# Performance work log

Measured on AMD Instinct MI355X. Metric: run time of the kernel, lower is better.

Reference implementation:

```python
import jax, jax.numpy as jnp
import numpy as np

NEG_SLOPE = 0.01  # torch leaky_relu default

def _leaky_relu(x):
    return jnp.where(x >= 0, x, NEG_SLOPE * x)

def setup_inputs() -> dict:
    key = jax.random.key(0)
    ks = jax.random.split(key, 12)
    n_drug, n_disease, n_edges, d = 10000, 10000, 1000000, 100
    inp = {
        "x_drug": jax.random.normal(ks[0], (n_drug, d), dtype=jnp.float32),
        "x_disease": jax.random.normal(ks[1], (n_disease, d), dtype=jnp.float32),
        "edge_label_index": jax.random.randint(ks[2], (2, n_edges), 0, n_drug, dtype=jnp.int64),
        "W1": jax.random.normal(ks[3], (200, 128), dtype=jnp.float32) * 0.07,
        "b1": jax.random.normal(ks[4], (128,), dtype=jnp.float32) * 0.01,
        "W2": jax.random.normal(ks[5], (128, 32), dtype=jnp.float32) * 0.09,
        "b2": jax.random.normal(ks[6], (32,), dtype=jnp.float32) * 0.01,
        "W3": jax.random.normal(ks[7], (32, 16), dtype=jnp.float32) * 0.18,
        "b3": jax.random.normal(ks[8], (16,), dtype=jnp.float32) * 0.01,
        "W4": jax.random.normal(ks[9], (16, 1), dtype=jnp.float32) * 0.25,
        "b4": jax.random.normal(ks[10], (1,), dtype=jnp.float32) * 0.01,
    }
    return inp

def reference(x_drug, x_disease, edge_label_index, W1, b1, W2, b2, W3, b3, W4, b4):
    # gather per-edge node embeddings and concat -> [E, 200]
    ef = jnp.concatenate([x_drug[edge_label_index[0]],
                          x_disease[edge_label_index[1]]], axis=-1)
    ef = _leaky_relu(ef @ W1 + b1)
    ef = _leaky_relu(ef @ W2 + b2)
    ef = _leaky_relu(ef @ W3 + b3)
    ef = ef @ W4 + b4
    return jnp.squeeze(ef, axis=-1)
```

## Files before the change

kernel.cpp:

```cpp
#include <hip/hip_runtime.h>
#include <cstdint>
#include <cstddef>

typedef _Float16 hf2   __attribute__((ext_vector_type(2)));
typedef _Float16 f16x8 __attribute__((ext_vector_type(8)));
typedef float    f32x4 __attribute__((ext_vector_type(4)));

__device__ __forceinline__ hf2 u2h(unsigned u) { union { unsigned u; hf2 h; } c; c.u = u; return c.h; }
__device__ __forceinline__ unsigned h2u(hf2 h) { union { hf2 h; unsigned u; } c; c.h = h; return c.u; }
__device__ __forceinline__ f16x8 q2h8(uint4 q) { union { uint4 q; f16x8 h; } c; c.q = q; return c.h; }

__device__ __forceinline__ hf2 pkrtz(float lo, float hi) {
    auto v = __builtin_amdgcn_cvt_pkrtz(lo, hi);
    union { decltype(v) a; hf2 b; } c; c.a = v; return c.b;
}
__device__ __forceinline__ float lreluf(float x) { return fmaxf(x, 0.01f * x); }
__device__ __forceinline__ unsigned lr2(unsigned a, unsigned b) {
    hf2 s = u2h(a) + u2h(b);
    hf2 m = s * (_Float16)0.01f;
    hf2 r = __builtin_elementwise_max(s, m);
    return h2u(r);
}

__global__ __launch_bounds__(256) void node_proj2(
    const float* __restrict__ xd, const float* __restrict__ xi,
    const float* __restrict__ W1, const float* __restrict__ b1,
    _Float16* __restrict__ Pd, _Float16* __restrict__ Pi,
    int nd, int ni, int nblk_d, int nblk_i,
    const float* __restrict__ W2, const float* __restrict__ W3,
    const float* __restrict__ W4,
    _Float16* __restrict__ W2f, unsigned* __restrict__ W3p,
    unsigned* __restrict__ W4p,
    const unsigned* __restrict__ ew, long long nwords, int* __restrict__ flag)
{
    const int t = threadIdx.x;
    const int nproj = nblk_d + nblk_i;

    if ((int)blockIdx.x >= nproj) {
        if ((int)blockIdx.x == nproj) {
            for (int idx = t; idx < 4096; idx += 256) {
                int i  = idx & 7;
                int l  = (idx >> 3) & 63;
                int kt = (idx >> 9) & 3;
                int nt = (idx >> 11) & 1;
                int k = kt * 32 + 8 * (l >> 4) + i;
                int j = nt * 16 + (l & 15);
                W2f[idx] = (_Float16)W2[k * 32 + j];
            }
            for (int idx = t; idx < 256; idx += 256) {
                int kp = idx >> 4, j = idx & 15;
                W3p[idx] = h2u(pkrtz(W3[(2 * kp) * 16 + j], W3[(2 * kp + 1) * 16 + j]));
            }
            if (t < 8) W4p[t] = h2u(pkrtz(W4[2 * t], W4[2 * t + 1]));
        } else if (t < 64) {
            const long long pairs = nwords / 2;
            const long long step  = pairs / 64;
            unsigned v = 0;
            for (int s = 0; s < 4; ++s) {
                long long p = (long long)t * step + (long long)s * (step / 4 + 1);
                if (p < pairs) v |= ew[2 * p + 1];
            }
            unsigned long long ball = __ballot(v != 0);
            if (t == 0) *flag = (ball == 0ULL) ? 1 : 0;
        }
        return;
    }

    __shared__ float xs[1600];
    const int c  = t & 127;
    const int ty = t >> 7;
    const bool dis = (int)blockIdx.x >= nblk_d;
    const int b = dis ? (blockIdx.x - nblk_d) : blockIdx.x;
    const int n = dis ? ni : nd;
    const float* x = dis ? xi : xd;
    const float* W = dis ? (W1 + 100 * 128) : W1;
    _Float16* P = dis ? Pi : Pd;
    const float bv = dis ? b1[c] : 0.f;
    const int r0 = b * 16;

    const long long gbase = (long long)r0 * 100;
    const long long lim   = (long long)n * 100;
    for (int idx = t; idx < 1600; idx += 256) {
        long long g = gbase + idx;
        xs[idx] = (g < lim) ? x[g] : 0.f;
    }
    __syncthreads();

    float acc[8];
#pragma unroll
    for (int i = 0; i < 8; ++i) acc[i] = bv;

    const float4* xs4 = (const float4*)xs;
#pragma unroll 5
    for (int kk = 0; kk < 25; ++kk) {
        float w0 = W[(4 * kk + 0) * 128 + c];
        float w1 = W[(4 * kk + 1) * 128 + c];
        float w2 = W[(4 * kk + 2) * 128 + c];
        float w3 = W[(4 * kk + 3) * 128 + c];
#pragma unroll
        for (int i = 0; i < 8; ++i) {
            float4 xv = xs4[(ty * 8 + i) * 25 + kk];
            acc[i] = fmaf(xv.x, w0, acc[i]);
            acc[i] = fmaf(xv.y, w1, acc[i]);
            acc[i] = fmaf(xv.z, w2, acc[i]);
            acc[i] = fmaf(xv.w, w3, acc[i]);
        }
    }
#pragma unroll
    for (int i = 0; i < 8; ++i) {
        int r = r0 + ty * 8 + i;
        if (r < n) P[(size_t)r * 128 + c] = (_Float16)acc[i];
    }
}

__global__ __launch_bounds__(128) void edge_mlp(
    const void* __restrict__ eidx_raw,
    const _Float16* __restrict__ Pd, const _Float16* __restrict__ Pi,
    const _Float16* __restrict__ W2f, const float* __restrict__ b2,
    const unsigned* __restrict__ W3u, const float* __restrict__ b3,
    const unsigned* __restrict__ W4u, const float* __restrict__ b4,
    const int* __restrict__ flag64,
    float* __restrict__ out, int E)
{
    __shared__ __align__(16) _Float16 Hs[128 * 128];
    __shared__ int sidx[2][128];
    _Float16* H2 = Hs;

    const int t = threadIdx.x;
    const int l = t & 63;
    const int w = t >> 6;
    const int e_g = blockIdx.x * 128 + t;
    const int e_c = (e_g < E) ? e_g : (E - 1);

    int i0, i1;
    if (*flag64) {
        const long long* p = (const long long*)eidx_raw;
        i0 = (int)p[e_c];
        i1 = (int)p[(size_t)E + e_c];
    } else {
        const int* p = (const int*)eidx_raw;
        i0 = p[e_c];
        i1 = p[(size_t)E + e_c];
    }
    sidx[0][t] = i0;
    sidx[1][t] = i1;

    f16x8 bf[2][4];
    {
        const uint4* W2q = (const uint4*)W2f;
#pragma unroll
        for (int nt = 0; nt < 2; ++nt)
#pragma unroll
            for (int kt = 0; kt < 4; ++kt)
                bf[nt][kt] = q2h8(W2q[(nt * 4 + kt) * 64 + l]);
    }
    const float b2v0 = b2[l & 15];
    const float b2v1 = b2[16 + (l & 15)];
    __syncthreads();

    {
        const int c = t & 15;
        const int r = t >> 4;
        const uint4* Pdq = (const uint4*)Pd;
        const uint4* Piq = (const uint4*)Pi;
        uint4* Hq = (uint4*)Hs;
#pragma unroll
        for (int i = 0; i < 16; ++i) {
            const int e = i * 8 + r;
            uint4 A = Pdq[(size_t)sidx[0][e] * 16 + c];
            uint4 B = Piq[(size_t)sidx[1][e] * 16 + c];
            uint4 hv;
            hv.x = lr2(A.x, B.x);
            hv.y = lr2(A.y, B.y);
            hv.z = lr2(A.z, B.z);
            hv.w = lr2(A.w, B.w);
            Hq[e * 16 + (c ^ (e & 7))] = hv;
        }
    }
    __syncthreads();

    f32x4 acc2[4][2];
    {
        const uint4* Hq = (const uint4*)Hs;
        const int er = l & 15;
        const int cg = l >> 4;
#pragma unroll
        for (int q = 0; q < 4; ++q) {
            const int e = (w * 4 + q) * 16 + er;
#pragma unroll
            for (int nt = 0; nt < 2; ++nt) acc2[q][nt] = (f32x4){0.f, 0.f, 0.f, 0.f};
#pragma unroll
            for (int kt = 0; kt < 4; ++kt) {
                const int c = kt * 4 + cg;
                f16x8 af = q2h8(Hq[e * 16 + (c ^ (e & 7))]);
                acc2[q][0] = __builtin_amdgcn_mfma_f32_16x16x32_f16(af, bf[0][kt], acc2[q][0], 0, 0, 0);
                acc2[q][1] = __builtin_amdgcn_mfma_f32_16x16x32_f16(af, bf[1][kt], acc2[q][1], 0, 0, 0);
            }
        }
    }
    __syncthreads();

#pragma unroll
    for (int q = 0; q < 4; ++q) {
#pragma unroll
        for (int nt = 0; nt < 2; ++nt) {
            const float bb = nt ? b2v1 : b2v0;
            const int j = nt * 16 + (l & 15);
#pragma unroll
            for (int r = 0; r < 4; ++r) {
                const int e = (w * 4 + q) * 16 + (l >> 4) * 4 + r;
                H2[e * 34 + j] = (_Float16)lreluf(acc2[q][nt][r] + bb);
            }
        }
    }
    __syncthreads();

    const unsigned* H2u = (const unsigned*)H2;
    float a3[16];
#pragma unroll
    for (int j = 0; j < 16; ++j) a3[j] = b3[j];
#pragma unroll
    for (int kp = 0; kp < 16; ++kp) {
        hf2 hp = u2h(H2u[t * 17 + kp]);
#pragma unroll
        for (int j = 0; j < 16; ++j)
            a3[j] = __builtin_amdgcn_fdot2(hp, u2h(W3u[kp * 16 + j]), a3[j], false);
    }

    float o = b4[0];
#pragma unroll
    for (int kp = 0; kp < 8; ++kp) {
        hf2 hp = pkrtz(lreluf(a3[2 * kp]), lreluf(a3[2 * kp + 1]));
        o = __builtin_amdgcn_fdot2(hp, u2h(W4u[kp]), o, false);
    }

    if (e_g < E) out[e_g] = o;
}

extern "C" void kernel_launch(void* const* d_in, const int* in_sizes, int n_in,
                              void* d_out, int out_size, void* d_ws, size_t ws_size,
                              hipStream_t stream)
{
    const float* x_drug = (const float*)d_in[0];
    const float* x_dis  = (const float*)d_in[1];
    const void*  eidx   = d_in[2];
    const float* W1 = (const float*)d_in[3];
    const float* b1 = (const float*)d_in[4];
    const float* W2 = (const float*)d_in[5];
    const float* b2 = (const float*)d_in[6];
    const float* W3 = (const float*)d_in[7];
    const float* b3 = (const float*)d_in[8];
    const float* W4 = (const float*)d_in[9];
    const float* b4 = (const float*)d_in[10];

    const int nd = in_sizes[0] / 100;
    const int ni = in_sizes[1] / 100;
    const int E  = in_sizes[2] / 2;

    char* ws = (char*)d_ws;
    _Float16* Pd = (_Float16*)ws;                    size_t off = (size_t)nd * 128 * 2;
    _Float16* Pi = (_Float16*)(ws + off);            off += (size_t)ni * 128 * 2;
    _Float16* W2f = (_Float16*)(ws + off);           off += 4096 * 2;
    unsigned* W3p = (unsigned*)(ws + off);           off += 16 * 16 * 4;
    unsigned* W4p = (unsigned*)(ws + off);           off += 8 * 4;
    int* flag = (int*)(ws + off);

    const int nblk_d = (nd + 15) / 16;
    const int nblk_i = (ni + 15) / 16;

    node_proj2<<<nblk_d + nblk_i + 2, 256, 0, stream>>>(
        x_drug, x_dis, W1, b1, Pd, Pi, nd, ni, nblk_d, nblk_i,
        W2, W3, W4, W2f, W3p, W4p,
        (const unsigned*)eidx, 2LL * E, flag);

    edge_mlp<<<(E + 127) / 128, 128, 0, stream>>>(eidx, Pd, Pi,
                                                  W2f, b2, W3p, b3, W4p, b4,
                                                  flag, (float*)d_out, E);
}
```

Baseline: 144.9 us.

## Restructure edge MLP into single-wave blocks, gather directly into MFMA operands

The edge kernel now runs one 64-lane wave per block over 64 edges. Each 16-edge group gathers its projected node rows straight into MFMA A-operands, so the 32 KB shared staging buffer and the shared index arrays go away. Layer 3 becomes an MFMA with W3 pre-laid-out in fp16, and layer 4 is done by a cross-lane shuffle reduction instead of per-thread fdot2 loops. The aim is to cut shared-memory footprint and raise occupancy, at the cost of more global gathers issued per wave and a barrier per 16-edge group.

After: 161.4 us. 11.4% more time.

```diff
diff --git a/kernel.cpp b/kernel.cpp
--- a/kernel.cpp
+++ b/kernel.cpp
@@ -6,20 +6,16 @@
 typedef _Float16 f16x8 __attribute__((ext_vector_type(8)));
 typedef float    f32x4 __attribute__((ext_vector_type(4)));
 
-__device__ __forceinline__ hf2 u2h(unsigned u) { union { unsigned u; hf2 h; } c; c.u = u; return c.h; }
-__device__ __forceinline__ unsigned h2u(hf2 h) { union { hf2 h; unsigned u; } c; c.h = h; return c.u; }
 __device__ __forceinline__ f16x8 q2h8(uint4 q) { union { uint4 q; f16x8 h; } c; c.q = q; return c.h; }
-
 __device__ __forceinline__ hf2 pkrtz(float lo, float hi) {
     auto v = __builtin_amdgcn_cvt_pkrtz(lo, hi);
     union { decltype(v) a; hf2 b; } c; c.a = v; return c.b;
 }
 __device__ __forceinline__ float lreluf(float x) { return fmaxf(x, 0.01f * x); }
-__device__ __forceinline__ unsigned lr2(unsigned a, unsigned b) {
-    hf2 s = u2h(a) + u2h(b);
-    hf2 m = s * (_Float16)0.01f;
-    hf2 r = __builtin_elementwise_max(s, m);
-    return h2u(r);
+__device__ __forceinline__ f16x8 lrelu8(uint4 a, uint4 b) {
+    f16x8 s = q2h8(a) + q2h8(b);
+    f16x8 m = s * (_Float16)0.01f;
+    return __builtin_elementwise_max(s, m);
 }
 
 __global__ __launch_bounds__(256) void node_proj2(
@@ -28,9 +24,7 @@
     _Float16* __restrict__ Pd, _Float16* __restrict__ Pi,
     int nd, int ni, int nblk_d, int nblk_i,
     const float* __restrict__ W2, const float* __restrict__ W3,
-    const float* __restrict__ W4,
-    _Float16* __restrict__ W2f, unsigned* __restrict__ W3p,
-    unsigned* __restrict__ W4p,
+    _Float16* __restrict__ W2f, _Float16* __restrict__ W3f,
     const unsigned* __restrict__ ew, long long nwords, int* __restrict__ flag)
 {
     const int t = threadIdx.x;
@@ -47,11 +41,10 @@
                 int j = nt * 16 + (l & 15);
                 W2f[idx] = (_Float16)W2[k * 32 + j];
             }
-            for (int idx = t; idx < 256; idx += 256) {
-                int kp = idx >> 4, j = idx & 15;
-                W3p[idx] = h2u(pkrtz(W3[(2 * kp) * 16 + j], W3[(2 * kp + 1) * 16 + j]));
+            for (int idx = t; idx < 512; idx += 256) {
+                int i = idx & 7, l = idx >> 3;
+                W3f[idx] = (_Float16)W3[(8 * (l >> 4) + i) * 16 + (l & 15)];
             }
-            if (t < 8) W4p[t] = h2u(pkrtz(W4[2 * t], W4[2 * t + 1]));
         } else if (t < 64) {
             const long long pairs = nwords / 2;
             const long long step  = pairs / 64;
@@ -113,24 +106,22 @@
     }
 }
 
-__global__ __launch_bounds__(128) void edge_mlp(
+__global__ __launch_bounds__(64, 4) void edge_mlp(
     const void* __restrict__ eidx_raw,
     const _Float16* __restrict__ Pd, const _Float16* __restrict__ Pi,
     const _Float16* __restrict__ W2f, const float* __restrict__ b2,
-    const unsigned* __restrict__ W3u, const float* __restrict__ b3,
-    const unsigned* __restrict__ W4u, const float* __restrict__ b4,
+    const _Float16* __restrict__ W3f, const float* __restrict__ b3,
+    const float* __restrict__ W4, const float* __restrict__ b4,
     const int* __restrict__ flag64,
     float* __restrict__ out, int E)
 {
-    __shared__ __align__(16) _Float16 Hs[128 * 128];
-    __shared__ int sidx[2][128];
-    _Float16* H2 = Hs;
-
-    const int t = threadIdx.x;
-    const int l = t & 63;
-    const int w = t >> 6;
-    const int e_g = blockIdx.x * 128 + t;
-    const int e_c = (e_g < E) ? e_g : (E - 1);
+    __shared__ __align__(16) float H2[64 * 36];
+
+    const int l  = threadIdx.x;
+    const int er = l & 15;
+    const int cg = l >> 4;
+    const int base = blockIdx.x * 64;
+    const int e_c = min(base + l, E - 1);
 
     int i0, i1;
     if (*flag64) {
@@ -142,99 +133,71 @@
         i0 = p[e_c];
         i1 = p[(size_t)E + e_c];
     }
-    sidx[0][t] = i0;
-    sidx[1][t] = i1;
-
-    f16x8 bf[2][4];
+
+    f16x8 bf0[4], bf1[4];
     {
         const uint4* W2q = (const uint4*)W2f;
 #pragma unroll
-        for (int nt = 0; nt < 2; ++nt)
-#pragma unroll
-            for (int kt = 0; kt < 4; ++kt)
-                bf[nt][kt] = q2h8(W2q[(nt * 4 + kt) * 64 + l]);
-    }
-    const float b2v0 = b2[l & 15];
-    const float b2v1 = b2[16 + (l & 15)];
-    __syncthreads();
-
-    {
-        const int c = t & 15;
-        const int r = t >> 4;
-        const uint4* Pdq = (const uint4*)Pd;
-        const uint4* Piq = (const uint4*)Pi;
-        uint4* Hq = (uint4*)Hs;
-#pragma unroll
-        for (int i = 0; i < 16; ++i) {
-            const int e = i * 8 + r;
-            uint4 A = Pdq[(size_t)sidx[0][e] * 16 + c];
-            uint4 B = Piq[(size_t)sidx[1][e] * 16 + c];
-            uint4 hv;
-            hv.x = lr2(A.x, B.x);
-            hv.y = lr2(A.y, B.y);
-            hv.z = lr2(A.z, B.z);
-            hv.w = lr2(A.w, B.w);
-            Hq[e * 16 + (c ^ (e & 7))] = hv;
-        }
-    }
-    __syncthreads();
-
-    f32x4 acc2[4][2];
-    {
-        const uint4* Hq = (const uint4*)Hs;
-        const int er = l & 15;
-        const int cg = l >> 4;
-#pragma unroll
-        for (int q = 0; q < 4; ++q) {
-            const int e = (w * 4 + q) * 16 + er;
-#pragma unroll
-            for (int nt = 0; nt < 2; ++nt) acc2[q][nt] = (f32x4){0.f, 0.f, 0.f, 0.f};
-#pragma unroll
-            for (int kt = 0; kt < 4; ++kt) {
-                const int c = kt * 4 + cg;
-                f16x8 af = q2h8(Hq[e * 16 + (c ^ (e & 7))]);
-                acc2[q][0] = __builtin_amdgcn_mfma_f32_16x16x32_f16(af, bf[0][kt], acc2[q][0], 0, 0, 0);
-                acc2[q][1] = __builtin_amdgcn_mfma_f32_16x16x32_f16(af, bf[1][kt], acc2[q][1], 0, 0, 0);
-            }
-        }
-    }
-    __syncthreads();
+        for (int kt = 0; kt < 4; ++kt) {
+            bf0[kt] = q2h8(W2q[kt * 64 + l]);
+            bf1[kt] = q2h8(W2q[256 + kt * 64 + l]);
+        }
+    }
+    const f16x8 w3f = q2h8(((const uint4*)W3f)[l]);
+    const float  b2v0 = b2[er], b2v1 = b2[16 + er];
+    const float4 b3q  = ((const float4*)b3)[cg];
+    const float4 w4q  = ((const float4*)W4)[cg];
+    const float  b4v  = b4[0];
 
 #pragma unroll
     for (int q = 0; q < 4; ++q) {
-#pragma unroll
-        for (int nt = 0; nt < 2; ++nt) {
-            const float bb = nt ? b2v1 : b2v0;
-            const int j = nt * 16 + (l & 15);
-#pragma unroll
-            for (int r = 0; r < 4; ++r) {
-                const int e = (w * 4 + q) * 16 + (l >> 4) * 4 + r;
-                H2[e * 34 + j] = (_Float16)lreluf(acc2[q][nt][r] + bb);
-            }
-        }
-    }
-    __syncthreads();
-
-    const unsigned* H2u = (const unsigned*)H2;
-    float a3[16];
-#pragma unroll
-    for (int j = 0; j < 16; ++j) a3[j] = b3[j];
-#pragma unroll
-    for (int kp = 0; kp < 16; ++kp) {
-        hf2 hp = u2h(H2u[t * 17 + kp]);
-#pragma unroll
-        for (int j = 0; j < 16; ++j)
-            a3[j] = __builtin_amdgcn_fdot2(hp, u2h(W3u[kp * 16 + j]), a3[j], false);
-    }
-
-    float o = b4[0];
-#pragma unroll
-    for (int kp = 0; kp < 8; ++kp) {
-        hf2 hp = pkrtz(lreluf(a3[2 * kp]), lreluf(a3[2 * kp + 1]));
-        o = __builtin_amdgcn_fdot2(hp, u2h(W4u[kp]), o, false);
-    }
-
-    if (e_g < E) out[e_g] = o;
+        const int src = q * 16 + er;
+        const int j0 = __shfl(i0, src, 64);
+        const int j1 = __shfl(i1, src, 64);
+        const uint4* rowD = (const uint4*)(Pd + (size_t)j0 * 128);
+        const uint4* rowI = (const uint4*)(Pi + (size_t)j1 * 128);
+
+        f32x4 c0 = {0.f, 0.f, 0.f, 0.f}, c1 = {0.f, 0.f, 0.f, 0.f};
+#pragma unroll
+        for (int kt = 0; kt < 4; ++kt) {
+            f16x8 af = lrelu8(rowD[kt * 4 + cg], rowI[kt * 4 + cg]);
+            c0 = __builtin_amdgcn_mfma_f32_16x16x32_f16(af, bf0[kt], c0, 0, 0, 0);
+            c1 = __builtin_amdgcn_mfma_f32_16x16x32_f16(af, bf1[kt], c1, 0, 0, 0);
+        }
+
+#pragma unroll
+        for (int r = 0; r < 4; ++r) {
+            const int e = q * 16 + 4 * cg + r;
+            H2[e * 36 + er]      = lreluf(c0[r] + b2v0);
+            H2[e * 36 + 16 + er] = lreluf(c1[r] + b2v1);
+        }
+        __syncthreads();
+
+        const int e2 = q * 16 + er;
+        const float4* hr = (const float4*)&H2[e2 * 36 + 8 * cg];
+        float4 h0 = hr[0], h1 = hr[1];
+        union { hf2 h[4]; f16x8 v; } u;
+        u.h[0] = pkrtz(h0.x, h0.y);
+        u.h[1] = pkrtz(h0.z, h0.w);
+        u.h[2] = pkrtz(h1.x, h1.y);
+        u.h[3] = pkrtz(h1.z, h1.w);
+
+        f32x4 d3 = __builtin_amdgcn_mfma_f32_16x16x32_f16(
+            w3f, u.v, (f32x4){0.f, 0.f, 0.f, 0.f}, 0, 0, 0);
+
+        float v = lreluf(d3[0] + b3q.x) * w4q.x;
+        v      += lreluf(d3[1] + b3q.y) * w4q.y;
+        v      += lreluf(d3[2] + b3q.z) * w4q.z;
+        v      += lreluf(d3[3] + b3q.w) * w4q.w;
+        v += __shfl_xor(v, 16, 64);
+        v += __shfl_xor(v, 32, 64);
+
+        if (cg == 0) {
+            const int eo = base + q * 16 + er;
+            if (eo < E) out[eo] = v + b4v;
+        }
+        __syncthreads();
+    }
 }
 
 extern "C" void kernel_launch(void* const* d_in, const int* in_sizes, int n_in,
@@ -258,11 +221,10 @@
     const int E  = in_sizes[2] / 2;
 
     char* ws = (char*)d_ws;
-    _Float16* Pd = (_Float16*)ws;                    size_t off = (size_t)nd * 128 * 2;
-    _Float16* Pi = (_Float16*)(ws + off);            off += (size_t)ni * 128 * 2;
+    _Float16* Pd  = (_Float16*)ws;                   size_t off = (size_t)nd * 128 * 2;
+    _Float16* Pi  = (_Float16*)(ws + off);           off += (size_t)ni * 128 * 2;
     _Float16* W2f = (_Float16*)(ws + off);           off += 4096 * 2;
-    unsigned* W3p = (unsigned*)(ws + off);           off += 16 * 16 * 4;
-    unsigned* W4p = (unsigned*)(ws + off);           off += 8 * 4;
+    _Float16* W3f = (_Float16*)(ws + off);           off += 512 * 2;
     int* flag = (int*)(ws + off);
 
     const int nblk_d = (nd + 15) / 16;
@@ -270,10 +232,10 @@
 
     node_proj2<<<nblk_d + nblk_i + 2, 256, 0, stream>>>(
         x_drug, x_dis, W1, b1, Pd, Pi, nd, ni, nblk_d, nblk_i,
-        W2, W3, W4, W2f, W3p, W4p,
+        W2, W3, W2f, W3f,
         (const unsigned*)eidx, 2LL * E, flag);
 
-    edge_mlp<<<(E + 127) / 128, 128, 0, stream>>>(eidx, Pd, Pi,
-                                                  W2f, b2, W3p, b3, W4p, b4,
-                                                  flag, (float*)d_out, E);
-}
+    edge_mlp<<<(E + 63) / 64, 64, 0, stream>>>(eidx, Pd, Pi,
+                                               W2f, b2, W3f, b3, W4, b4,
+                                               flag, (float*)d_out, E);
+}
```
